# Optimization experiments

Hardware: AMD Instinct MI355X
Metric: run time of the kernel (lower is better)

## Reference

```python
import jax, jax.numpy as jnp
import numpy as np

EPS_KERNEL = 1e-4   # eps inside softmax_kernel exp
EPS_ATTN = 1e-6     # eps added to k_cumsum in infer_hidden_states
CHUNK = 128         # default chunk_size of infer_hidden_states
HEADS = 8


def softmax_kernel(data, proj, is_query):
    # Performer FAVOR+ softmax kernel feature map.
    dn = data.shape[-1] ** -0.25                 # data normalizer
    ratio = proj.shape[0] ** -0.5
    dd = jnp.einsum('bhnd,jd->bhnj', dn * data, proj)        # [b,h,n,f]
    diag = 0.5 * (dn ** 2) * jnp.sum(data * data, axis=-1, keepdims=True)
    if is_query:
        m = jnp.max(dd, axis=-1, keepdims=True)
    else:
        m = jnp.max(dd)
    return ratio * (jnp.exp(dd - diag - m) + EPS_KERNEL)


def setup_inputs() -> dict:
    key = jax.random.key(0)
    ks = jax.random.split(key, 6)
    b, n, dim, dh, nf = 2, 4096, 512, 64, 256
    sc = dim ** -0.5
    return {
        'x': jax.random.normal(ks[0], (b, n, dim), jnp.float32),
        'Wq': jax.random.normal(ks[1], (dim, dim), jnp.float32) * sc,
        'Wk': jax.random.normal(ks[2], (dim, dim), jnp.float32) * sc,
        'Wv': jax.random.normal(ks[3], (dim, dim), jnp.float32) * sc,
        'Wo': jax.random.normal(ks[4], (dim, dim), jnp.float32) * sc,
        'bo': jnp.zeros((dim,), jnp.float32),
        'proj': jax.random.normal(ks[5], (nf, dh), jnp.float32),
    }


def reference(x, Wq, Wk, Wv, Wo, bo, proj):
    b, n, dim = x.shape
    h = HEADS
    dh = dim // h
    def heads(t):
        return t.reshape(b, n, h, dh).transpose(0, 2, 1, 3)  # [b,h,n,dh]
    q = heads(x @ Wq.T)
    k = heads(x @ Wk.T)
    v = heads(x @ Wv.T)

    # feature maps (post_phi_layerPE=True, pos_emb=None)
    q = softmax_kernel(q, proj, True)    # [b,h,n,f]
    k = softmax_kernel(k, proj, False)   # [b,h,n,f]

    nc = n // CHUNK
    def to_chunks(t):
        f = t.shape[-1]
        return t.reshape(b, h, nc, CHUNK, f).transpose(2, 0, 1, 3, 4)  # [nc,b,h,c,f]
    qc, kc, vc = to_chunks(q), to_chunks(k), to_chunks(v)

    f = q.shape[-1]
    Z0 = jnp.zeros((b, h, 1, f), q.dtype)
    S0 = jnp.zeros((b, h, 1, f, dh), q.dtype)

    def step(carry, qkv):
        Z, S = carry
        qi, ki, vi = qkv                              # [b,h,c,*]
        k_cum = Z + jnp.cumsum(ki, axis=2)            # [b,h,c,f]
        D_inv = 1.0 / jnp.einsum('bhnd,bhnd->bhn', qi, k_cum + EPS_ATTN)
        ctx = jnp.einsum('bhnd,bhne->bhnde', ki, vi)  # [b,h,c,f,dh]
        ctx_cum = S + jnp.cumsum(ctx, axis=2)
        out = jnp.einsum('bhnde,bhnd,bhn->bhne', ctx_cum, qi, D_inv)
        return (k_cum[:, :, -1:], ctx_cum[:, :, -1:]), out

    (Zf, Sf), outs = jax.lax.scan(step, (Z0, S0), (qc, kc, vc))
    # outs: [nc,b,h,c,dh] -> [b,h,n,dh]
    out = outs.transpose(1, 2, 0, 3, 4).reshape(b, h, n, dh)
    out = out.transpose(0, 2, 1, 3).reshape(b, n, h * dh)
    out = out @ Wo.T + bo
    # states: Z=[b,h,f], S=[b,h,f,dh]
    return out, Zf[:, :, 0], Sf[:, :, 0]
```

## Files before the change

kernel.cpp:

```cpp
#include <hip/hip_runtime.h>
#include <hip/hip_bf16.h>

typedef unsigned short u16;
typedef unsigned int u32;
typedef __attribute__((ext_vector_type(8))) short bf16x8;
typedef __attribute__((ext_vector_type(4))) float f32x4;

#define LOG2E 1.4426950408889634f

__device__ __forceinline__ u16 f2bf(float f) {
    __hip_bfloat16 h = __float2bfloat16(f);
    u16 u; __builtin_memcpy(&u, &h, 2); return u;
}
__device__ __forceinline__ float bf2f(u16 h) { return __uint_as_float(((u32)h) << 16); }
__device__ __forceinline__ u32 pk(u16 a, u16 b) { return (u32)a | ((u32)b << 16); }
__device__ __forceinline__ int swz(int row, int col, int ld) {
    return ((row * ld + col) * 2) ^ ((row & 7) << 4);
}
__device__ __forceinline__ f32x4 MF(bf16x8 a, bf16x8 b, f32x4 c) {
    return __builtin_amdgcn_mfma_f32_16x16x32_bf16(a, b, c, 0, 0, 0);
}
__device__ __forceinline__ float wave_max(float v) {
    #pragma unroll
    for (int o = 32; o; o >>= 1) v = fmaxf(v, __shfl_xor(v, o));
    return v;
}
__device__ __forceinline__ void gload16(const void* g, void* l) {
    __builtin_amdgcn_global_load_lds(
        (const __attribute__((address_space(1))) void*)g,
        (__attribute__((address_space(3))) void*)l, 16, 0, 0);
}
__device__ __forceinline__ float gmax_decode(const u32* gmaxkey) {
    u32 key = *gmaxkey;
    u32 ub = (key & 0x80000000u) ? (key & 0x7fffffffu) : ~key;
    return __uint_as_float(ub);
}

template<bool ISB>
__global__ __launch_bounds__(256)
void conv_split(const float* __restrict__ src, u16* __restrict__ dst,
                int K, long total4, float scale)
{
    const int K4 = K >> 2;
    for (long i = (long)blockIdx.x * 256 + threadIdx.x; i < total4;
         i += (long)gridDim.x * 256) {
        long row = i / K4;
        int c = (int)(i - row * K4) * 4;
        float4 v = ((const float4*)src)[i];
        float a0 = v.x * scale, a1 = v.y * scale, a2 = v.z * scale, a3 = v.w * scale;
        u16 h0 = f2bf(a0), h1 = f2bf(a1), h2 = f2bf(a2), h3 = f2bf(a3);
        u16 l0 = f2bf(a0 - bf2f(h0)), l1 = f2bf(a1 - bf2f(h1));
        u16 l2 = f2bf(a2 - bf2f(h2)), l3 = f2bf(a3 - bf2f(h3));
        uint2 hh; hh.x = pk(h0, h1); hh.y = pk(h2, h3);
        uint2 ll; ll.x = pk(l0, l1); ll.y = pk(l2, l3);
        u16* d = dst + row * (3L * K) + c;
        *(uint2*)d = hh;
        *(uint2*)(d + (ISB ? 2 * K : K)) = hh;
        *(uint2*)(d + (ISB ? K : 2 * K)) = ll;
    }
}

__global__ __launch_bounds__(256)
void conv_plain(const float* __restrict__ src, u16* __restrict__ dst, long total4)
{
    for (long i = (long)blockIdx.x * 256 + threadIdx.x; i < total4;
         i += (long)gridDim.x * 256) {
        float4 v = ((const float4*)src)[i];
        ushort4 o;
        o.x = f2bf(v.x); o.y = f2bf(v.y); o.z = f2bf(v.z); o.w = f2bf(v.w);
        ((ushort4*)dst)[i] = o;
    }
}

__global__ __launch_bounds__(256)
void conv_w4(const float* __restrict__ Wq, const float* __restrict__ Wk,
             const float* __restrict__ Wv, const float* __restrict__ Wo,
             u16* __restrict__ Wqkvs, u16* __restrict__ Wos)
{
    const int seg = blockIdx.x >> 6;
    const float* src = seg == 0 ? Wq : (seg == 1 ? Wk : (seg == 2 ? Wv : Wo));
    u16* dst = (seg == 3) ? Wos : (Wqkvs + (size_t)seg * 262144);
    long i = (long)(blockIdx.x & 63) * 256 + threadIdx.x;
    for (; i < 65536L; i += 16384L) {
        float4 v = ((const float4*)src)[i];
        ushort4 o;
        o.x = f2bf(v.x); o.y = f2bf(v.y); o.z = f2bf(v.z); o.w = f2bf(v.w);
        ((ushort4*)dst)[i] = o;
    }
}

__global__ __launch_bounds__(256, 3)
void qkv_gemm(const u16* __restrict__ A, const u16* __restrict__ B,
              u16* __restrict__ qs, float* __restrict__ diagb,
              u16* __restrict__ Vtb)
{
    __shared__ char smem[34816];
    char* As = smem; char* Bs = smem + 16384;
    const int m0 = blockIdx.x * 128, by = blockIdx.y, n0 = by * 128;
    const int tid = threadIdx.x, lane = tid & 63, wave = tid >> 6;
    const int wm = (wave >> 1) * 64, wn = (wave & 1) * 64;
    const int fr = lane & 15, fk = (lane >> 4) * 8;
    const int lr8 = lane >> 3;
    const int cE = ((lane & 7) ^ lr8) << 3;
    f32x4 acc[4][4] = {};
    for (int k0 = 0; k0 < 512; k0 += 64) {
        #pragma unroll
        for (int t = 0; t < 4; t++) {
            int i = wave * 4 + t;
            int r = (i << 3) + lr8;
            gload16(A + (size_t)(m0 + r) * 512 + k0 + cE, As + (i << 10));
            gload16(B + (size_t)(n0 + r) * 512 + k0 + cE, Bs + (i << 10));
        }
        __syncthreads();
        #pragma unroll
        for (int ks = 0; ks < 2; ks++) {
            bf16x8 af[4], bfv[4];
            #pragma unroll
            for (int mf = 0; mf < 4; mf++)
                af[mf] = *(bf16x8*)(As + swz(wm + mf * 16 + fr, ks * 32 + fk, 64));
            #pragma unroll
            for (int nf = 0; nf < 4; nf++)
                bfv[nf] = *(bf16x8*)(Bs + swz(wn + nf * 16 + fr, ks * 32 + fk, 64));
            #pragma unroll
            for (int mf = 0; mf < 4; mf++)
                #pragma unroll
                for (int nf = 0; nf < 4; nf++)
                    acc[mf][nf] = MF(af[mf], bfv[nf], acc[mf][nf]);
        }
        __syncthreads();
    }
    const float dn = 0.35355339059327373f;
    const int sel = by >> 2;
    float* st = (float*)smem;
    for (int half = 0; half < 2; half++) {
        __syncthreads();
        if ((wave >> 1) == half) {
            #pragma unroll
            for (int mf = 0; mf < 4; mf++) {
                int lr = mf * 16 + (lane >> 4) * 4;
                #pragma unroll
                for (int nf = 0; nf < 4; nf++) {
                    int col = wn + nf * 16 + fr;
                    #pragma unroll
                    for (int r = 0; r < 4; r++)
                        st[(lr + r) * 130 + col] = acc[mf][nf][r];
                }
            }
        }
        __syncthreads();
        if (sel < 2) {
            int grow = m0 + half * 64 + (tid >> 2);
            int hl = (tid >> 1) & 1, e0 = (tid & 1) * 32;
            int h = (by & 3) * 2 + hl;
            alignas(16) u16 hbuf[32], lbuf[32];
            float ss = 0.f;
            #pragma unroll
            for (int q = 0; q < 32; q++) {
                float v = dn * st[(tid >> 2) * 130 + hl * 64 + e0 + q];
                ss += v * v;
                u16 hh = f2bf(v); hbuf[q] = hh; lbuf[q] = f2bf(v - bf2f(hh));
            }
            ss += __shfl_xor(ss, 1);
            if ((tid & 1) == 0)
                diagb[(size_t)sel * 65536 + grow * 8 + h] = 0.5f * LOG2E * ss;
            u16* d = qs + (size_t)sel * 12582912 + (size_t)grow * 1536 + h * 192 + e0;
            #pragma unroll
            for (int q = 0; q < 4; q++) *(uint4*)(d + q * 8) = *(uint4*)&hbuf[q * 8];
            #pragma unroll
            for (int q = 0; q < 4; q++) *(uint4*)(d + 64 + q * 8) = *(uint4*)&hbuf[q * 8];
            #pragma unroll
            for (int q = 0; q < 4; q++) *(uint4*)(d + 128 + q * 8) = *(uint4*)&lbuf[q * 8];
        } else {
            const int bb = blockIdx.x >> 5, cc2 = blockIdx.x & 31;
            int e_full = tid >> 1;
            int h_local = e_full >> 6;
            int e = e_full & 63;
            int rhalf = (tid & 1) * 32;
            int gc = (bb * 8 + (by & 3) * 2 + h_local) * 32 + cc2;
            alignas(16) u16 hbuf[32], lbuf[32];
            #pragma unroll
            for (int q = 0; q < 32; q++) {
                float v = st[(rhalf + q) * 130 + h_local * 64 + e];
                u16 hh = f2bf(v); hbuf[q] = hh; lbuf[q] = f2bf(v - bf2f(hh));
            }
            u16* dh = Vtb + (size_t)gc * 16384 + (size_t)e * 128 + half * 64 + rhalf;
            u16* dl = dh + 8192;
            #pragma unroll
            for (int q = 0; q < 4; q++) *(uint4*)(dh + q * 8) = *(uint4*)&hbuf[q * 8];
            #pragma unroll
            for (int q = 0; q < 4; q++) *(uint4*)(dl + q * 8) = *(uint4*)&lbuf[q * 8];
        }
    }
}

__global__ __launch_bounds__(256, 3)
void dd_gemm(const u16* __restrict__ Aq, const u16* __restrict__ Ak,
             const u16* __restrict__ Bp,
             const float* __restrict__ diagb, u32* __restrict__ gmax,
             u16* __restrict__ phiQ, u16* __restrict__ psiK)
{
    __shared__ char sm_[42240];
    char* As = sm_;
    char* Bs = sm_ + 8192;
    float* red  = (float*)(sm_ + 40960);
    float* srow = (float*)(sm_ + 41984);
    const int isq = (blockIdx.z < 8);
    const int h = isq ? blockIdx.z : (blockIdx.z - 8);
    const int m0 = blockIdx.x * 64;
    const u16* Ag = (isq ? Aq : Ak) + (size_t)m0 * 1536 + h * 192;
    const int tid = threadIdx.x, lane = tid & 63, wave = tid >> 6;
    const int wn = wave * 64;
    const int fr = lane & 15, fk = (lane >> 4) * 8;
    const int lr8 = lane >> 3;
    const int cE = ((lane & 7) ^ lr8) << 3;
    f32x4 acc[4][4] = {};
    for (int k0 = 0; k0 < 192; k0 += 64) {
        #pragma unroll
        for (int t = 0; t < 2; t++) {
            int i = wave * 2 + t;
            int r = (i << 3) + lr8;
            gload16(Ag + (size_t)r * 1536 + k0 + cE, As + (i << 10));
        }
        #pragma unroll
        for (int t = 0; t < 8; t++) {
            int i = wave * 8 + t;
            int r = (i << 3) + lr8;
            gload16(Bp + (size_t)r * 192 + k0 + cE, Bs + (i << 10));
        }
        __syncthreads();
        #pragma unroll
        for (int ks = 0; ks < 2; ks++) {
            bf16x8 af[4], bf4[4];
            #pragma unroll
            for (int mf = 0; mf < 4; mf++)
                af[mf] = *(bf16x8*)(As + swz(mf * 16 + fr, ks * 32 + fk, 64));
            #pragma unroll
            for (int nf = 0; nf < 4; nf++)
                bf4[nf] = *(bf16x8*)(Bs + swz(wn + nf * 16 + fr, ks * 32 + fk, 64));
            #pragma unroll
            for (int mf = 0; mf < 4; mf++)
                #pragma unroll
                for (int nf = 0; nf < 4; nf++)
                    acc[mf][nf] = MF(af[mf], bf4[nf], acc[mf][nf]);
        }
        __syncthreads();
    }

    if (!isq) {
        float mx = -1e30f;
        #pragma unroll
        for (int mf = 0; mf < 4; mf++)
            #pragma unroll
            for (int nf = 0; nf < 4; nf++)
                #pragma unroll
                for (int r = 0; r < 4; r++) mx = fmaxf(mx, acc[mf][nf][r]);
        mx = wave_max(mx);
        __syncthreads();
        if (lane == 0) red[wave] = mx;
        __syncthreads();
        if (tid == 0) {
            float m4 = fmaxf(fmaxf(red[0], red[1]), fmaxf(red[2], red[3]));
            u32 u = __float_as_uint(m4);
            u32 key = (u & 0x80000000u) ? ~u : (u | 0x80000000u);
            atomicMax(gmax, key);
        }
        if (tid < 64)
            srow[tid] = diagb[65536 + (size_t)(m0 + tid) * 8 + h];
    } else {
        float rm[4][4];
        #pragma unroll
        for (int mf = 0; mf < 4; mf++)
            #pragma unroll
            for (int r = 0; r < 4; r++) {
                float m = acc[mf][0][r];
                m = fmaxf(m, acc[mf][1][r]);
                m = fmaxf(m, acc[mf][2][r]);
                m = fmaxf(m, acc[mf][3][r]);
                #pragma unroll
                for (int o = 1; o < 16; o <<= 1) m = fmaxf(m, __shfl_xor(m, o));
                rm[mf][r] = m;
            }
        __syncthreads();
        if ((lane & 15) == 0) {
            #pragma unroll
            for (int mf = 0; mf < 4; mf++)
                #pragma unroll
                for (int r = 0; r < 4; r++)
                    red[(mf * 16 + (lane >> 4) * 4 + r) * 4 + wave] = rm[mf][r];
        }
        __syncthreads();
        if (tid < 64) {
            float m4 = fmaxf(fmaxf(red[tid * 4], red[tid * 4 + 1]),
                             fmaxf(red[tid * 4 + 2], red[tid * 4 + 3]));
            srow[tid] = m4 + diagb[(size_t)(m0 + tid) * 8 + h];
        }
    }
    u16* stg = (u16*)sm_;
    __syncthreads();
    #pragma unroll
    for (int mf = 0; mf < 4; mf++)
        #pragma unroll
        for (int r = 0; r < 4; r++) {
            int row = mf * 16 + (lane >> 4) * 4 + r;
            float s = srow[row];
            #pragma unroll
            for (int nf = 0; nf < 4; nf++) {
                float v = acc[mf][nf][r];
                u16 o = isq ? f2bf(0.0625f * (exp2f(v - s) + 1e-4f))
                            : f2bf(exp2f(v - s));
                stg[row * 264 + wn + nf * 16 + fr] = o;
            }
        }
    __syncthreads();
    {
        int lr = tid >> 2, c0 = (tid & 3) * 64;
        u16* base = isq ? phiQ : psiK;
        u16* dst = base + (size_t)(m0 + lr) * 2048 + h * 256 + c0;
        #pragma unroll
        for (int q = 0; q < 8; q++)
            *(uint4*)(dst + q * 8) = *(uint4*)(stg + lr * 264 + c0 + q * 8);
    }
}

__global__ __launch_bounds__(256)
void transpose_k(const u16* __restrict__ phiK, u16* __restrict__ phiKT)
{
    __shared__ u16 tr[64 * 136];
    const int gc = blockIdx.x, c = gc & 31, bh = gc >> 5, b = bh >> 3, h = bh & 7;
    const int row0 = b * 4096 + c * 128;
    const u16* src = phiK + (size_t)row0 * 2048 + h * 256;
    u16* dst = phiKT + (size_t)gc * 32768;
    const int tid = threadIdx.x;
    for (int f0 = 0; f0 < 256; f0 += 64) {
        #pragma unroll
        for (int j = 0; j < 4; j++) {
            int ci = tid + j * 256; int r = ci >> 3, ff = (ci & 7) * 8;
            bf16x8 w = *(const bf16x8*)(src + (size_t)r * 2048 + f0 + ff);
            #pragma unroll
            for (int q = 0; q < 8; q++) tr[(ff + q) * 136 + r] = (u16)w[q];
        }
        __syncthreads();
        {
            int f = tid >> 2, r0 = (tid & 3) * 32;
            uint4 a0 = *(uint4*)&tr[f * 136 + r0];
            uint4 a1 = *(uint4*)&tr[f * 136 + r0 + 8];
            uint4 a2 = *(uint4*)&tr[f * 136 + r0 + 16];
            uint4 a3 = *(uint4*)&tr[f * 136 + r0 + 24];
            u16* dp = dst + (size_t)(f0 + f) * 128 + r0;
            *(uint4*)dp = a0; *(uint4*)(dp + 8) = a1;
            *(uint4*)(dp + 16) = a2; *(uint4*)(dp + 24) = a3;
        }
        __syncthreads();
    }
}

__global__ __launch_bounds__(256, 3)
void proj_gemm(const u16* __restrict__ A, const u16* __restrict__ B,
               float* __restrict__ C, const float* __restrict__ bias)
{
    __shared__ char smem[34816];
    char* As = smem; char* Bs = smem + 16384;
    const int m0 = blockIdx.x * 128, n0 = blockIdx.y * 128;
    const int tid = threadIdx.x, lane = tid & 63, wave = tid >> 6;
    const int wm = (wave >> 1) * 64, wn = (wave & 1) * 64;
    const int fr = lane & 15, fk = (lane >> 4) * 8;
    const int lr8 = lane >> 3;
    const int cE = ((lane & 7) ^ lr8) << 3;
    f32x4 acc[4][4] = {};
    for (int k0 = 0; k0 < 512; k0 += 64) {
        #pragma unroll
        for (int t = 0; t < 4; t++) {
            int i = wave * 4 + t;
            int r = (i << 3) + lr8;
            gload16(A + (size_t)(m0 + r) * 512 + k0 + cE, As + (i << 10));
            gload16(B + (size_t)(n0 + r) * 512 + k0 + cE, Bs + (i << 10));
        }
        __syncthreads();
        #pragma unroll
        for (int ks = 0; ks < 2; ks++) {
            bf16x8 af[4], bfv[4];
            #pragma unroll
            for (int mf = 0; mf < 4; mf++)
                af[mf] = *(bf16x8*)(As + swz(wm + mf * 16 + fr, ks * 32 + fk, 64));
            #pragma unroll
            for (int nf = 0; nf < 4; nf++)
                bfv[nf] = *(bf16x8*)(Bs + swz(wn + nf * 16 + fr, ks * 32 + fk, 64));
            #pragma unroll
            for (int mf = 0; mf < 4; mf++)
                #pragma unroll
                for (int nf = 0; nf < 4; nf++)
                    acc[mf][nf] = MF(af[mf], bfv[nf], acc[mf][nf]);
        }
        __syncthreads();
    }
    float* st = (float*)smem;
    for (int half = 0; half < 2; half++) {
        __syncthreads();
        if ((wave >> 1) == half) {
            #pragma unroll
            for (int mf = 0; mf < 4; mf++) {
                int lr = mf * 16 + (lane >> 4) * 4;
                #pragma unroll
                for (int nf = 0; nf < 4; nf++) {
                    int col = wn + nf * 16 + fr;
                    #pragma unroll
                    for (int r = 0; r < 4; r++)
                        st[(lr + r) * 130 + col] = acc[mf][nf][r];
                }
            }
        }
        __syncthreads();
        int lr = tid >> 2, c0 = (tid & 3) * 32;
        int grow = m0 + half * 64 + lr;
        float* dst = C + (size_t)grow * 512 + n0 + c0;
        #pragma unroll
        for (int q = 0; q < 8; q++) {
            float4 v;
            v.x = st[lr * 130 + c0 + q * 4 + 0] + bias[n0 + c0 + q * 4 + 0];
            v.y = st[lr * 130 + c0 + q * 4 + 1] + bias[n0 + c0 + q * 4 + 1];
            v.z = st[lr * 130 + c0 + q * 4 + 2] + bias[n0 + c0 + q * 4 + 2];
            v.w = st[lr * 130 + c0 + q * 4 + 3] + bias[n0 + c0 + q * 4 + 3];
            *(float4*)(dst + q * 4) = v;
        }
    }
}

__global__ __launch_bounds__(256)
void chunk_sums_mfma(const u16* __restrict__ phiKT, const u16* __restrict__ Vt,
                     const u32* __restrict__ gmaxkey,
                     float* __restrict__ sbuf, float* __restrict__ zbuf)
{
    __shared__ char smem[49152];
    __shared__ float vcs[64];
    char* bufA = smem;
    char* bufBh = smem + 32768;
    char* bufBl = smem + 40960;
    const float mg = gmax_decode(gmaxkey);
    const float aF = 0.0625f * exp2f(-mg);
    const float bF = 0.0625f * 1e-4f;
    const int gc = blockIdx.x;
    const u16* Ag = phiKT + (size_t)gc * 32768;
    const u16* Bg = Vt + (size_t)gc * 16384;
    const int tid = threadIdx.x, lane = tid & 63, wave = tid >> 6;
    const int fr = lane & 15, fk = (lane >> 4) * 8;
    const int lr8 = lane >> 3;
    const int cE = ((lane & 7) ^ lr8) << 3;
    {
        float z = 0.f;
        const u16* zp = Ag + (size_t)tid * 128;
        #pragma unroll
        for (int j = 0; j < 16; j++) {
            bf16x8 w = *(const bf16x8*)(zp + j * 8);
            #pragma unroll
            for (int q = 0; q < 8; q++) z += bf2f((u16)w[q]);
        }
        zbuf[(size_t)gc * 256 + tid] = aF * z + bF * 128.0f;
    }
    if (tid < 64) {
        const u16* vh = Bg + (size_t)tid * 128;
        const u16* vl = vh + 8192;
        float s = 0.f;
        #pragma unroll
        for (int j = 0; j < 16; j++) {
            bf16x8 wh = *(const bf16x8*)(vh + j * 8);
            bf16x8 wl = *(const bf16x8*)(vl + j * 8);
            #pragma unroll
            for (int q = 0; q < 8; q++)
                s += bf2f((u16)wh[q]) + bf2f((u16)wl[q]);
        }
        vcs[tid] = s;
    }
    f32x4 acc[4][4] = {};
    for (int kh = 0; kh < 2; kh++) {
        #pragma unroll
        for (int t = 0; t < 8; t++) {
            int i = wave * 8 + t;
            int f = (i << 3) + lr8;
            gload16(Ag + (size_t)f * 128 + kh * 64 + cE, bufA + (i << 10));
        }
        #pragma unroll
        for (int t = 0; t < 2; t++) {
            int i = wave * 2 + t;
            int e = (i << 3) + lr8;
            gload16(Bg + (size_t)e * 128 + kh * 64 + cE, bufBh + (i << 10));
            gload16(Bg + 8192 + (size_t)e * 128 + kh * 64 + cE, bufBl + (i << 10));
        }
        __syncthreads();
        #pragma unroll
        for (int ks = 0; ks < 2; ks++) {
            bf16x8 af[4], bh4[4], bl4[4];
            #pragma unroll
            for (int mf = 0; mf < 4; mf++)
                af[mf] = *(bf16x8*)(bufA + swz(wave * 64 + mf * 16 + fr, ks * 32 + fk, 64));
            #pragma unroll
            for (int nf = 0; nf < 4; nf++) {
                bh4[nf] = *(bf16x8*)(bufBh + swz(nf * 16 + fr, ks * 32 + fk, 64));
                bl4[nf] = *(bf16x8*)(bufBl + swz(nf * 16 + fr, ks * 32 + fk, 64));
            }
            #pragma unroll
            for (int mf = 0; mf < 4; mf++)
                #pragma unroll
                for (int nf = 0; nf < 4; nf++) {
                    acc[mf][nf] = MF(af[mf], bh4[nf], acc[mf][nf]);
                    acc[mf][nf] = MF(af[mf], bl4[nf], acc[mf][nf]);
                }
        }
        __syncthreads();
    }
    #pragma unroll
    for (int mf = 0; mf < 4; mf++) {
        int fb = wave * 64 + mf * 16 + (lane >> 4) * 4;
        #pragma unroll
        for (int nf = 0; nf < 4; nf++) {
            int e = nf * 16 + fr;
            float vb = bF * vcs[e];
            #pragma unroll
            for (int r = 0; r < 4; r++)
                sbuf[(size_t)gc * 16384 + (size_t)(fb + r) * 64 + e] =
                    aF * acc[mf][nf][r] + vb;
        }
    }
}

__global__ __launch_bounds__(256)
void prefix_scan(const float* __restrict__ sbuf, const float* __restrict__ zbuf,
                 u16* __restrict__ SpT, float* __restrict__ Zp,
                 float* __restrict__ outZ, float* __restrict__ outS)
{
    __shared__ float trans[64 * 17];
    const int bh = blockIdx.x >> 4, f0 = (blockIdx.x & 15) * 16;
    const int tid = threadIdx.x;
    const int e_ = tid >> 2, fl = (tid & 3) * 4;
    float run[4] = {0.f, 0.f, 0.f, 0.f};
    float zrun = 0.f;
    for (int c = 0; c < 32; c++) {
        const int gc = bh * 32 + c;
        const float* base = sbuf + (size_t)gc * 16384 + f0 * 64;
        float v[4];
        #pragma unroll
        for (int i = 0; i < 4; i++) v[i] = base[tid + i * 256];
        #pragma unroll
        for (int i = 0; i < 4; i++) {
            int idx = tid + i * 256;
            trans[(idx & 63) * 17 + (idx >> 6)] = run[i];
        }
        float zv = 0.f;
        if (tid < 16) zv = zbuf[(size_t)gc * 256 + f0 + tid];
        __syncthreads();
        {
            alignas(8) u16 hb[4], lb[4];
            #pragma unroll
            for (int q = 0; q < 4; q++) {
                float vv = trans[e_ * 17 + fl + q];
                u16 hh = f2bf(vv); hb[q] = hh; lb[q] = f2bf(vv - bf2f(hh));
            }
            u16* dh = SpT + (size_t)gc * 32768 + e_ * 256 + f0 + fl;
            *(uint2*)dh = *(uint2*)hb;
            *(uint2*)(dh + 16384) = *(uint2*)lb;
        }
        if (tid < 16) { Zp[(size_t)gc * 256 + f0 + tid] = zrun; zrun += zv; }
        #pragma unroll
        for (int i = 0; i < 4; i++) run[i] += v[i];
        __syncthreads();
    }
    #pragma unroll
    for (int i = 0; i < 4; i++)
        outS[(size_t)bh * 16384 + f0 * 64 + tid + i * 256] = run[i];
    if (tid < 16) outZ[bh * 256 + f0 + tid] = zrun;
}

__global__ __launch_bounds__(256)
void chunk_out_mfma(const u16* __restrict__ phiQ, const u16* __restrict__ psiK,
                    const u16* __restrict__ Vt, const u16* __restrict__ SpT,
                    const float* __restrict__ Zp, const u32* __restrict__ gmaxkey,
                    u16* __restrict__ aouts)
{
    extern __shared__ char sm[];
    char* bufQ = sm;
    char* bufK = sm + 16384;
    char* bufA = sm + 32768;
    float* Dl = (float*)(sm + 65536);
    float* Zl = (float*)(sm + 66048);
    float* RowQ = (float*)(sm + 66304);
    const float mg = gmax_decode(gmaxkey);
    const float aF = 0.0625f * exp2f(-mg);
    const float bF = 0.0625f * 1e-4f;
    const int gc = blockIdx.x, c = gc & 31, bh = gc >> 5, b = bh >> 3, h = bh & 7;
    const int row0 = b * 4096 + c * 128;
    const u16* Qg = phiQ + (size_t)row0 * 2048 + h * 256;
    const u16* Kg = psiK + (size_t)row0 * 2048 + h * 256;
    const u16* Vg = Vt + (size_t)gc * 16384;
    const u16* Sg = SpT + (size_t)gc * 32768;
    const float* Zg = Zp + (size_t)gc * 256;
    const int tid = threadIdx.x, lane = tid & 63, wave = tid >> 6;
    const int fr = lane & 15, fk = (lane >> 4) * 8;
    const int dr = tid >> 1, dc = (tid & 1) * 32;
    const int lr8 = lane >> 3;
    const int cE = ((lane & 7) ^ lr8) << 3;

    f32x4 acc2[2][8] = {};
    f32x4 acc1[2][4] = {};
    float dotZ = 0.f, sumQ = 0.f;

    for (int f0 = 0; f0 < 256; f0 += 64) {
        #pragma unroll
        for (int t = 0; t < 4; t++) {
            int i = wave * 4 + t;
            int r = (i << 3) + lr8;
            gload16(Qg + (size_t)r * 2048 + f0 + cE, bufQ + (i << 10));
            gload16(Kg + (size_t)r * 2048 + f0 + cE, bufK + (i << 10));
        }
        #pragma unroll
        for (int t = 0; t < 2; t++) {
            int i = wave * 2 + t;
            int e = (i << 3) + lr8;
            gload16(Sg + (size_t)e * 256 + f0 + cE, bufA + (i << 10));
            gload16(Sg + 16384 + (size_t)e * 256 + f0 + cE, bufA + 8192 + (i << 10));
        }
        if (tid < 64) Zl[tid] = Zg[f0 + tid];
        __syncthreads();
        #pragma unroll
        for (int ks = 0; ks < 2; ks++) {
            bf16x8 af[2];
            af[0] = *(bf16x8*)(bufQ + swz(wave * 32 + fr, ks * 32 + fk, 64));
            af[1] = *(bf16x8*)(bufQ + swz(wave * 32 + 16 + fr, ks * 32 + fk, 64));
            #pragma unroll
            for (int nf = 0; nf < 8; nf++) {
                bf16x8 bv = *(bf16x8*)(bufK + swz(nf * 16 + fr, ks * 32 + fk, 64));
                acc2[0][nf] = MF(af[0], bv, acc2[0][nf]);
                acc2[1][nf] = MF(af[1], bv, acc2[1][nf]);
            }
            #pragma unroll
            for (int nf = 0; nf < 4; nf++) {
                bf16x8 bvh = *(bf16x8*)(bufA + swz(nf * 16 + fr, ks * 32 + fk, 64));
                bf16x8 bvl = *(bf16x8*)(bufA + 8192 + swz(nf * 16 + fr, ks * 32 + fk, 64));
                acc1[0][nf] = MF(af[0], bvh, acc1[0][nf]);
                acc1[1][nf] = MF(af[1], bvh, acc1[1][nf]);
                acc1[0][nf] = MF(af[0], bvl, acc1[0][nf]);
                acc1[1][nf] = MF(af[1], bvl, acc1[1][nf]);
            }
        }
        #pragma unroll
        for (int jj = 0; jj < 4; jj++) {
            bf16x8 qv = *(bf16x8*)(bufQ + swz(dr, dc + jj * 8, 64));
            f32x4 z0 = *(f32x4*)(Zl + dc + jj * 8);
            f32x4 z1 = *(f32x4*)(Zl + dc + jj * 8 + 4);
            #pragma unroll
            for (int q = 0; q < 8; q++) {
                float qf = bf2f((u16)qv[q]);
                sumQ += qf;
                dotZ += qf * (q < 4 ? z0[q] : z1[q - 4]);
            }
        }
        __syncthreads();
    }
    {
        float rq = sumQ + __shfl_xor(sumQ, 1);
        if ((tid & 1) == 0) RowQ[dr] = rq;
    }
    __syncthreads();
    float4 vvh[4];
    #pragma unroll
    for (int j = 0; j < 4; j++) {
        int ci = tid + j * 256; int e = ci >> 4, cc = (ci & 15) * 8;
        vvh[j] = *(const float4*)(Vg + (size_t)e * 128 + cc);
    }
    #pragma unroll
    for (int mf = 0; mf < 2; mf++) {
        int rb = wave * 32 + mf * 16 + (lane >> 4) * 4;
        #pragma unroll
        for (int nf = 0; nf < 8; nf++) {
            int col = nf * 16 + fr;
            #pragma unroll
            for (int r = 0; r < 4; r++) {
                float v = (col <= rb + r) ? (aF * acc2[mf][nf][r] + bF * RowQ[rb + r]) : 0.f;
                *(u16*)(bufA + swz(rb + r, col, 128)) = f2bf(v);
            }
        }
    }
    #pragma unroll
    for (int j = 0; j < 4; j++) {
        int ci = tid + j * 256; int e = ci >> 4, cc = (ci & 15) * 8;
        *(float4*)(bufK + swz(e, cc, 128)) = vvh[j];
    }
    __syncthreads();
    {
        const int dcA = (tid & 1) * 64;
        float rs = 0.f;
        #pragma unroll
        for (int jj = 0; jj < 8; jj++) {
            bf16x8 av = *(bf16x8*)(bufA + swz(dr, dcA + jj * 8, 128));
            #pragma unroll
            for (int q = 0; q < 8; q++) rs += bf2f((u16)av[q]);
        }
        float tot = rs + dotZ + 1e-6f * sumQ;
        tot += __shfl_xor(tot, 1);
        if ((tid & 1) == 0) Dl[dr] = tot;
    }
    #pragma unroll
    for (int ks = 0; ks < 4; ks++) {
        bf16x8 af[2];
        af[0] = *(bf16x8*)(bufA + swz(wave * 32 + fr, ks * 32 + fk, 128));
        af[1] = *(bf16x8*)(bufA + swz(wave * 32 + 16 + fr, ks * 32 + fk, 128));
        #pragma unroll
        for (int nf = 0; nf < 4; nf++) {
            bf16x8 bvh = *(bf16x8*)(bufK + swz(nf * 16 + fr, ks * 32 + fk, 128));
            acc1[0][nf] = MF(af[0], bvh, acc1[0][nf]);
            acc1[1][nf] = MF(af[1], bvh, acc1[1][nf]);
        }
    }
    __syncthreads();
    float* st = (float*)sm;
    #pragma unroll
    for (int mf = 0; mf < 2; mf++) {
        int rb = wave * 32 + mf * 16 + (lane >> 4) * 4;
        #pragma unroll
        for (int r = 0; r < 4; r++) {
            float dinv = 1.f / Dl[rb + r];
            #pragma unroll
            for (int nf = 0; nf < 4; nf++)
                st[(rb + r) * 65 + nf * 16 + fr] = acc1[mf][nf][r] * dinv;
        }
    }
    __syncthreads();
    {
        int lr = tid >> 1, e0 = (tid & 1) * 32;
        alignas(16) u16 hb[32];
        #pragma unroll
        for (int q = 0; q < 32; q++) hb[q] = f2bf(st[lr * 65 + e0 + q]);
        u16* d = aouts + (size_t)(row0 + lr) * 512 + h * 64 + e0;
        #pragma unroll
        for (int q = 0; q < 4; q++) *(uint4*)(d + q * 8) = *(uint4*)&hb[q * 8];
    }
}

extern "C" void kernel_launch(void* const* d_in, const int* in_sizes, int n_in,
                              void* d_out, int out_size, void* d_ws, size_t ws_size,
                              hipStream_t stream)
{
    const float* x    = (const float*)d_in[0];
    const float* Wq   = (const float*)d_in[1];
    const float* Wk   = (const float*)d_in[2];
    const float* Wv   = (const float*)d_in[3];
    const float* Wo   = (const float*)d_in[4];
    const float* bo   = (const float*)d_in[5];
    const float* proj = (const float*)d_in[6];
    float* out = (float*)d_out;
    float* ws = (float*)d_ws;

    float* diagb = ws + 4194304;
    u16*   phi   = (u16*)(ws + 12582912);
    u16*   Vtb   = (u16*)(ws + 37748736);
    float* sbuf  = ws + 41943040;
    u16*   qs    = (u16*)(ws + 41943040);
    u16*   phiKT = (u16*)(ws + 50331648);
    u16*   SpT   = (u16*)(ws + 50331648);
    u16*   xs    = (u16*)(ws + 58720256);
    u16*   aouts = xs;
    u16*   Wqkvs = (u16*)(ws + 65011712);
    float* zbuf  = ws + 65142784;
    float* Zp    = ws + 65273856;
    u32*   gmax  = (u32*)(ws + 65404928);
    u16*   Wos   = (u16*)(ws + 66191360);
    u16*   projs = (u16*)(ws + 66584576);

    float* outO = out;
    float* outZ = out + 4194304;
    float* outS = out + 4198400;

    dim3 blk(256);

    conv_plain<<<1024, blk, 0, stream>>>(x, xs, 1048576L);
    conv_w4<<<256, blk, 0, stream>>>(Wq, Wk, Wv, Wo, Wqkvs, Wos);
    conv_split<true ><<<16, blk, 0, stream>>>(proj, projs, 64, 4096L, LOG2E);
    qkv_gemm<<<dim3(64, 12), blk, 0, stream>>>(xs, Wqkvs, qs, diagb, Vtb);
    hipMemsetAsync(gmax, 0, 4, stream);
    const u16* ksplit = qs + 12582912;
    u16* psiK = phi + (size_t)8192 * 2048;
    dd_gemm<<<dim3(128, 1, 16), blk, 0, stream>>>(qs, ksplit, projs, diagb, gmax,
                                                  phi, psiK);
    transpose_k<<<512, blk, 0, stream>>>(psiK, phiKT);
    chunk_sums_mfma<<<512, blk, 0, stream>>>(phiKT, Vtb, gmax, sbuf, zbuf);
    prefix_scan<<<256, blk, 0, stream>>>(sbuf, zbuf, SpT, Zp, outZ, outS);
    hipFuncSetAttribute((const void*)chunk_out_mfma,
                        hipFuncAttributeMaxDynamicSharedMemorySize, 66816);
    chunk_out_mfma<<<512, blk, 66816, stream>>>(phi, psiK, Vtb, SpT, Zp, gmax, aouts);
    proj_gemm<<<dim3(64, 4), blk, 0, stream>>>(aouts, Wos, outO, bo);
}
```

Measured before the change: 208.4 us.

## Fuse K feature transpose into dd_gemm and drop duplicated hi split copy

The separate transpose_k kernel is removed, and dd_gemm now writes the transposed psiK tile straight from its shared-memory staging buffer, saving a kernel launch and a full read and write of psiK. The split Q/K buffer shrinks from three 64-wide segments (hi, hi, lo) to two (hi, lo). dd_gemm reuses the hi tile already in shared memory for the second K step instead of loading a duplicate copy, which cuts global traffic in qkv_gemm and dd_gemm. In exchange, the transposed store reads LDS column-wise and adds work to the K blocks of dd_gemm.

New measurement: 198.4 us. -4.8%, faster.

```diff
diff --git a/kernel.cpp b/kernel.cpp
--- a/kernel.cpp
+++ b/kernel.cpp
@@ -163,13 +163,11 @@
             ss += __shfl_xor(ss, 1);
             if ((tid & 1) == 0)
                 diagb[(size_t)sel * 65536 + grow * 8 + h] = 0.5f * LOG2E * ss;
-            u16* d = qs + (size_t)sel * 12582912 + (size_t)grow * 1536 + h * 192 + e0;
+            u16* d = qs + (size_t)sel * 8388608 + (size_t)grow * 1024 + h * 128 + e0;
             #pragma unroll
             for (int q = 0; q < 4; q++) *(uint4*)(d + q * 8) = *(uint4*)&hbuf[q * 8];
             #pragma unroll
-            for (int q = 0; q < 4; q++) *(uint4*)(d + 64 + q * 8) = *(uint4*)&hbuf[q * 8];
-            #pragma unroll
-            for (int q = 0; q < 4; q++) *(uint4*)(d + 128 + q * 8) = *(uint4*)&lbuf[q * 8];
+            for (int q = 0; q < 4; q++) *(uint4*)(d + 64 + q * 8) = *(uint4*)&lbuf[q * 8];
         } else {
             const int bb = blockIdx.x >> 5, cc2 = blockIdx.x & 31;
             int e_full = tid >> 1;
@@ -197,7 +195,8 @@
 void dd_gemm(const u16* __restrict__ Aq, const u16* __restrict__ Ak,
              const u16* __restrict__ Bp,
              const float* __restrict__ diagb, u32* __restrict__ gmax,
-             u16* __restrict__ phiQ, u16* __restrict__ psiK)
+             u16* __restrict__ phiQ, u16* __restrict__ psiK,
+             u16* __restrict__ psiKT)
 {
     __shared__ char sm_[42240];
     char* As = sm_;
@@ -207,25 +206,28 @@
     const int isq = (blockIdx.z < 8);
     const int h = isq ? blockIdx.z : (blockIdx.z - 8);
     const int m0 = blockIdx.x * 64;
-    const u16* Ag = (isq ? Aq : Ak) + (size_t)m0 * 1536 + h * 192;
+    const u16* Ag = (isq ? Aq : Ak) + (size_t)m0 * 1024 + h * 128;
     const int tid = threadIdx.x, lane = tid & 63, wave = tid >> 6;
     const int wn = wave * 64;
     const int fr = lane & 15, fk = (lane >> 4) * 8;
     const int lr8 = lane >> 3;
     const int cE = ((lane & 7) ^ lr8) << 3;
     f32x4 acc[4][4] = {};
-    for (int k0 = 0; k0 < 192; k0 += 64) {
-        #pragma unroll
-        for (int t = 0; t < 2; t++) {
-            int i = wave * 2 + t;
-            int r = (i << 3) + lr8;
-            gload16(Ag + (size_t)r * 1536 + k0 + cE, As + (i << 10));
+    for (int kk = 0; kk < 3; kk++) {
+        if (kk != 1) {
+            int aoff = kk ? 64 : 0;
+            #pragma unroll
+            for (int t = 0; t < 2; t++) {
+                int i = wave * 2 + t;
+                int r = (i << 3) + lr8;
+                gload16(Ag + (size_t)r * 1024 + aoff + cE, As + (i << 10));
+            }
         }
         #pragma unroll
         for (int t = 0; t < 8; t++) {
             int i = wave * 8 + t;
             int r = (i << 3) + lr8;
-            gload16(Bp + (size_t)r * 192 + k0 + cE, Bs + (i << 10));
+            gload16(Bp + (size_t)r * 192 + kk * 64 + cE, Bs + (i << 10));
         }
         __syncthreads();
         #pragma unroll
@@ -320,37 +322,21 @@
         for (int q = 0; q < 8; q++)
             *(uint4*)(dst + q * 8) = *(uint4*)(stg + lr * 264 + c0 + q * 8);
     }
-}
-
-__global__ __launch_bounds__(256)
-void transpose_k(const u16* __restrict__ phiK, u16* __restrict__ phiKT)
-{
-    __shared__ u16 tr[64 * 136];
-    const int gc = blockIdx.x, c = gc & 31, bh = gc >> 5, b = bh >> 3, h = bh & 7;
-    const int row0 = b * 4096 + c * 128;
-    const u16* src = phiK + (size_t)row0 * 2048 + h * 256;
-    u16* dst = phiKT + (size_t)gc * 32768;
-    const int tid = threadIdx.x;
-    for (int f0 = 0; f0 < 256; f0 += 64) {
-        #pragma unroll
-        for (int j = 0; j < 4; j++) {
-            int ci = tid + j * 256; int r = ci >> 3, ff = (ci & 7) * 8;
-            bf16x8 w = *(const bf16x8*)(src + (size_t)r * 2048 + f0 + ff);
-            #pragma unroll
-            for (int q = 0; q < 8; q++) tr[(ff + q) * 136 + r] = (u16)w[q];
-        }
-        __syncthreads();
-        {
-            int f = tid >> 2, r0 = (tid & 3) * 32;
-            uint4 a0 = *(uint4*)&tr[f * 136 + r0];
-            uint4 a1 = *(uint4*)&tr[f * 136 + r0 + 8];
-            uint4 a2 = *(uint4*)&tr[f * 136 + r0 + 16];
-            uint4 a3 = *(uint4*)&tr[f * 136 + r0 + 24];
-            u16* dp = dst + (size_t)(f0 + f) * 128 + r0;
-            *(uint4*)dp = a0; *(uint4*)(dp + 8) = a1;
-            *(uint4*)(dp + 16) = a2; *(uint4*)(dp + 24) = a3;
-        }
-        __syncthreads();
+    if (!isq) {
+        const int bb = m0 >> 12, cch = (m0 >> 7) & 31, rc0 = m0 & 64;
+        const int gc = ((bb * 8 + h) << 5) + cch;
+        u16* dT = psiKT + (size_t)gc * 32768 + (size_t)tid * 128 + rc0;
+        #pragma unroll
+        for (int jj = 0; jj < 4; jj++) {
+            u32 w[8];
+            #pragma unroll
+            for (int p = 0; p < 8; p++) {
+                int r = jj * 16 + p * 2;
+                w[p] = pk(stg[r * 264 + tid], stg[(r + 1) * 264 + tid]);
+            }
+            *(uint4*)(dT + jj * 16) = *(uint4*)&w[0];
+            *(uint4*)(dT + jj * 16 + 8) = *(uint4*)&w[4];
+        }
     }
 }
 
@@ -770,16 +756,15 @@
 
     dim3 blk(256);
 
+    hipMemsetAsync(gmax, 0, 4, stream);
     conv_plain<<<1024, blk, 0, stream>>>(x, xs, 1048576L);
     conv_w4<<<256, blk, 0, stream>>>(Wq, Wk, Wv, Wo, Wqkvs, Wos);
     conv_split<true ><<<16, blk, 0, stream>>>(proj, projs, 64, 4096L, LOG2E);
     qkv_gemm<<<dim3(64, 12), blk, 0, stream>>>(xs, Wqkvs, qs, diagb, Vtb);
-    hipMemsetAsync(gmax, 0, 4, stream);
-    const u16* ksplit = qs + 12582912;
+    const u16* ksplit = qs + 8388608;
     u16* psiK = phi + (size_t)8192 * 2048;
     dd_gemm<<<dim3(128, 1, 16), blk, 0, stream>>>(qs, ksplit, projs, diagb, gmax,
-                                                  phi, psiK);
-    transpose_k<<<512, blk, 0, stream>>>(psiK, phiKT);
+                                                  phi, psiK, phiKT);
     chunk_sums_mfma<<<512, blk, 0, stream>>>(phiKT, Vtb, gmax, sbuf, zbuf);
     prefix_scan<<<256, blk, 0, stream>>>(sbuf, zbuf, SpT, Zp, outZ, outS);
     hipFuncSetAttribute((const void*)chunk_out_mfma,
```
